# Optimization experiments

Hardware: AMD Instinct MI355X
Metric: run time of the kernel (lower is better)

The kernel has to match this reference:

```python
import jax, jax.numpy as jnp
import numpy as np

NEG_SLOPE = 0.2  # PyG GATConv leaky_relu slope


def _embed(feats, W1, b1, W2, b2, Wc, bc):
    # collapse_esm (two plain Linears, no activation) then linear_comb
    esm = feats[..., 24:] @ W1 + b1
    esm = esm @ W2 + b2
    x = jnp.concatenate([feats[..., :24], esm], axis=-1)
    return x @ Wc + bc


def _gat_conv(x, src, dst, n, W, a_src, a_dst, b, concat):
    # PyG GATConv: project, per-edge attention logits, softmax over incoming edges at dst,
    # weighted scatter-sum. Self loops already included in (src, dst).
    H, C = a_src.shape
    h = (x @ W).reshape(-1, H, C)                 # [N,H,C]
    s = (h * a_src).sum(-1)                       # [N,H]
    d = (h * a_dst).sum(-1)                       # [N,H]
    e = jax.nn.leaky_relu(s[src] + d[dst], NEG_SLOPE)  # [E,H]
    m = jax.ops.segment_max(e, dst, num_segments=n)
    e = jnp.exp(e - m[dst])
    z = jax.ops.segment_sum(e, dst, num_segments=n)
    alpha = e / z[dst]                            # [E,H]
    out = jax.ops.segment_sum(h[src] * alpha[:, :, None], dst, num_segments=n)  # [N,H,C]
    out = out.reshape(n, H * C) if concat else out.mean(axis=1)
    return out + b


def setup_inputs() -> dict:
    key = jax.random.key(0)
    ks = jax.random.split(key, 24)
    N, E, B, F = 100000, 3200000, 8, 50
    NF, M1, M2, M3, CH = 1304, 652, 326, 350, 32
    L, H, HID = 3, 8, 4
    f32 = jnp.float32
    inp = {
        "node_features": jax.random.normal(ks[0], (N, NF), f32),
        "edge_index": jax.random.randint(ks[1], (2, E), 0, N, dtype=jnp.int32),
        "edge_attr": jax.random.normal(ks[2], (E, 8), f32),
        "frag_emb": jax.random.normal(ks[3], (B, F, NF), f32),
        "W_esm1": jax.random.normal(ks[4], (NF - 24, M1), f32) / np.sqrt(NF - 24),
        "b_esm1": jnp.zeros((M1,), f32),
        "W_esm2": jax.random.normal(ks[5], (M1, M2), f32) / np.sqrt(M1),
        "b_esm2": jnp.zeros((M2,), f32),
        "W_comb": jax.random.normal(ks[6], (M3, CH), f32) / np.sqrt(M3),
        "b_comb": jnp.zeros((CH,), f32),
        "gat1_W": jax.random.normal(ks[7], (L, CH, H * HID), f32) / np.sqrt(CH),
        "gat1_asrc": jax.random.normal(ks[8], (L, H, HID), f32) * 0.1,
        "gat1_adst": jax.random.normal(ks[9], (L, H, HID), f32) * 0.1,
        "gat1_b": jnp.zeros((L, H * HID), f32),
        "gat2_W": jax.random.normal(ks[10], (L, H * HID, CH), f32) / np.sqrt(H * HID),
        "gat2_asrc": jax.random.normal(ks[11], (L, 1, CH), f32) * 0.1,
        "gat2_adst": jax.random.normal(ks[12], (L, 1, CH), f32) * 0.1,
        "gat2_b": jnp.zeros((L, CH), f32),
        "W_fin": jax.random.normal(ks[13], (CH, 1), f32) / np.sqrt(CH),
        "b_fin": jnp.zeros((1,), f32),
    }
    return inp


def reference(node_features, edge_index, edge_attr, frag_emb,
              W_esm1, b_esm1, W_esm2, b_esm2, W_comb, b_comb,
              gat1_W, gat1_asrc, gat1_adst, gat1_b,
              gat2_W, gat2_asrc, gat2_adst, gat2_b,
              W_fin, b_fin):
    N = node_features.shape[0]
    loop = jnp.arange(N, dtype=edge_index.dtype)
    src = jnp.concatenate([edge_index[0], loop])  # self loops (PyG default)
    dst = jnp.concatenate([edge_index[1], loop])

    x = _embed(node_features, W_esm1, b_esm1, W_esm2, b_esm2, W_comb, b_comb)  # [N,32]
    for i in range(gat1_W.shape[0]):
        x = _gat_conv(x, src, dst, N, gat1_W[i], gat1_asrc[i], gat1_adst[i], gat1_b[i], True)
        x = jax.nn.elu(x)
        x = _gat_conv(x, src, dst, N, gat2_W[i], gat2_asrc[i], gat2_adst[i], gat2_b[i], False)

    ys = _embed(frag_emb, W_esm1, b_esm1, W_esm2, b_esm2, W_comb, b_comb)  # [B,F,32]
    B, F, C = ys.shape
    xb = x.reshape(B, N // B, C)                      # equal-size graphs
    A = jax.nn.softmax(jnp.einsum('bnd,bfd->bnf', xb, ys), axis=-1)
    p = jnp.einsum('bnf,bfd->bnd', A, ys)             # [B,n,32]
    return jax.nn.sigmoid(p @ W_fin + b_fin).squeeze(-1)  # [B,n]
```

## Files before the change

### kernel.cpp

```cpp
#include <hip/hip_runtime.h>
#include <hip/hip_bf16.h>

#define NF 1304
#define M1 652
#define M2 326
#define CH 32
#define NHEAD1 8
#define HID1 4
#define NLAYER 3
#define FRAG 50
#define NBATCH 8
#define DPAD 32

static inline int ceil_div(int a, int b){ return (a + b - 1)/b; }

__device__ __forceinline__ unsigned short f2h(float f){
  _Float16 h = (_Float16)f;
  unsigned short u;
  __builtin_memcpy(&u, &h, 2);
  return u;
}
__device__ __forceinline__ float h2f(unsigned short u){
  _Float16 h;
  __builtin_memcpy(&h, &u, 2);
  return (float)h;
}

#define TM 64
#define TN 64
#define TKK 16
__global__ __launch_bounds__(256) void gemm_bias(
    const float* __restrict__ A, int lda,
    const float* __restrict__ B, int ldb,
    const float* __restrict__ bias,
    float* __restrict__ C, int ldc,
    int M, int N, int K, int acc)
{
  __shared__ float As[TKK][TM + 1];
  __shared__ float Bs[TKK][TN];
  int tid = threadIdx.x;
  int tx = tid & 15, ty = tid >> 4;
  int row0 = blockIdx.y * TM, col0 = blockIdx.x * TN;
  float c[4][4] = {};
  for (int k0 = 0; k0 < K; k0 += TKK) {
    #pragma unroll
    for (int p = 0; p < 4; ++p) {
      int r = (tid >> 4) + p * 16;
      int kk = tid & 15;
      int gr = row0 + r, gk = k0 + kk;
      float v = 0.f;
      if (gr < M && gk < K) v = A[(long long)gr * lda + gk];
      As[kk][r] = v;
    }
    #pragma unroll
    for (int p = 0; p < 4; ++p) {
      int kk = (tid >> 6) + p * 4;
      int cc = tid & 63;
      int gk = k0 + kk, gc = col0 + cc;
      float v = 0.f;
      if (gk < K && gc < N) v = B[(long long)gk * ldb + gc];
      Bs[kk][cc] = v;
    }
    __syncthreads();
    #pragma unroll
    for (int kk = 0; kk < TKK; ++kk) {
      float a[4], b[4];
      #pragma unroll
      for (int i = 0; i < 4; ++i) a[i] = As[kk][ty + 16 * i];
      #pragma unroll
      for (int j = 0; j < 4; ++j) b[j] = Bs[kk][tx + 16 * j];
      #pragma unroll
      for (int i = 0; i < 4; ++i)
        #pragma unroll
        for (int j = 0; j < 4; ++j)
          c[i][j] += a[i] * b[j];
    }
    __syncthreads();
  }
  #pragma unroll
  for (int i = 0; i < 4; ++i) {
    int gr = row0 + ty + 16 * i;
    if (gr >= M) continue;
    #pragma unroll
    for (int j = 0; j < 4; ++j) {
      int gc = col0 + tx + 16 * j;
      if (gc >= N) continue;
      float v = c[i][j];
      if (bias) v += bias[gc];
      if (acc) v += C[(long long)gr * ldc + gc];
      C[(long long)gr * ldc + gc] = v;
    }
  }
}

__global__ void fold_misc_kernel(const float* __restrict__ Wc, const float* __restrict__ T1,
                                 const float* __restrict__ b1, const float* __restrict__ b2,
                                 const float* __restrict__ bc,
                                 float* __restrict__ Wbig, float* __restrict__ bfold)
{
  int tid = threadIdx.x;
  for (int i = tid; i < 24 * CH; i += 256) Wbig[i] = Wc[i];
  if (tid < CH) {
    float v = bc[tid];
    for (int k = 0; k < M2; ++k) v += b2[k] * Wc[(24 + k) * CH + tid];
    for (int i = 0; i < M1; ++i) v += b1[i] * T1[i * CH + tid];
    bfold[tid] = v;
  }
}

#define EK 64
__global__ __launch_bounds__(256) void gemm_n32(
    const float* __restrict__ A, int M, int K,
    const float* __restrict__ W, const float* __restrict__ bias,
    float* __restrict__ C)
{
  __shared__ float As[64][65];
  __shared__ float Ws[EK][32];
  int tid = threadIdx.x;
  int row0 = blockIdx.x * 64;
  int tx = tid & 7, ty = tid >> 3;
  float c0[4] = {}, c1[4] = {};
  for (int k0 = 0; k0 < K; k0 += EK) {
    #pragma unroll
    for (int p = 0; p < 4; ++p) {
      int q = tid + p * 256;
      int r = q >> 4, c4 = (q & 15) * 4;
      int gr = row0 + r, gk = k0 + c4;
      float4 v = make_float4(0.f, 0.f, 0.f, 0.f);
      if (gr < M) {
        if (gk + 3 < K) v = *(const float4*)&A[(long long)gr * K + gk];
        else {
          float t[4] = {0.f, 0.f, 0.f, 0.f};
          for (int i = 0; i < 4; ++i) if (gk + i < K) t[i] = A[(long long)gr * K + gk + i];
          v = make_float4(t[0], t[1], t[2], t[3]);
        }
      }
      As[r][c4 + 0] = v.x; As[r][c4 + 1] = v.y; As[r][c4 + 2] = v.z; As[r][c4 + 3] = v.w;
    }
    #pragma unroll
    for (int p = 0; p < 2; ++p) {
      int q = tid + p * 256;
      int r = q >> 3, c4 = (q & 7) * 4;
      int gk = k0 + r;
      float4 v = make_float4(0.f, 0.f, 0.f, 0.f);
      if (gk < K) v = *(const float4*)&W[(long long)gk * 32 + c4];
      *(float4*)&Ws[r][c4] = v;
    }
    __syncthreads();
    #pragma unroll
    for (int kk = 0; kk < EK; ++kk) {
      float4 b = *(const float4*)&Ws[kk][tx * 4];
      float a0 = As[ty * 2][kk], a1 = As[ty * 2 + 1][kk];
      c0[0] += a0 * b.x; c0[1] += a0 * b.y; c0[2] += a0 * b.z; c0[3] += a0 * b.w;
      c1[0] += a1 * b.x; c1[1] += a1 * b.y; c1[2] += a1 * b.z; c1[3] += a1 * b.w;
    }
    __syncthreads();
  }
  float4 bb = *(const float4*)&bias[tx * 4];
  int gr0 = row0 + ty * 2;
  if (gr0 < M) {
    float4 v = make_float4(c0[0] + bb.x, c0[1] + bb.y, c0[2] + bb.z, c0[3] + bb.w);
    *(float4*)&C[(long long)gr0 * 32 + tx * 4] = v;
  }
  if (gr0 + 1 < M) {
    float4 v = make_float4(c1[0] + bb.x, c1[1] + bb.y, c1[2] + bb.z, c1[3] + bb.w);
    *(float4*)&C[(long long)(gr0 + 1) * 32 + tx * 4] = v;
  }
}

__global__ void zero_deg_kernel(int* __restrict__ degp, long long n)
{
  long long i = (long long)blockIdx.x * 256 + threadIdx.x;
  if (i < n) degp[i] = 0;
}
__global__ void rank_kernel(const int* __restrict__ ei, int E,
                            int* __restrict__ degp, int* __restrict__ rank)
{
  int e = blockIdx.x * 256 + threadIdx.x;
  if (e < E) rank[e] = atomicAdd(&degp[(long long)ei[E + e] * DPAD], 1);
}
__global__ void partial_kernel(const int* __restrict__ degp, int N, int* __restrict__ partial)
{
  __shared__ int sd[256];
  int i = blockIdx.x * 256 + threadIdx.x;
  sd[threadIdx.x] = (i < N) ? degp[(long long)i * DPAD] : 0;
  __syncthreads();
  for (int off = 128; off > 0; off >>= 1) {
    if (threadIdx.x < off) sd[threadIdx.x] += sd[threadIdx.x + off];
    __syncthreads();
  }
  if (threadIdx.x == 0) partial[blockIdx.x] = sd[0];
}
__global__ void scanp_kernel(int* __restrict__ partial, int NB)
{
  __shared__ int sd[512];
  int t = threadIdx.x;
  int v = (t < NB) ? partial[t] : 0;
  sd[t] = v;
  __syncthreads();
  for (int off = 1; off < 512; off <<= 1) {
    int u = (t >= off) ? sd[t - off] : 0;
    __syncthreads();
    sd[t] += u;
    __syncthreads();
  }
  if (t < NB) partial[t] = sd[t] - v;
}
__global__ void scan_final_kernel(const int* __restrict__ degp, int N,
                                  const int* __restrict__ partial,
                                  int* __restrict__ rowptr)
{
  __shared__ int sd[256];
  int i = blockIdx.x * 256 + threadIdx.x;
  int t = threadIdx.x;
  int v = (i < N) ? degp[(long long)i * DPAD] : 0;
  sd[t] = v;
  __syncthreads();
  for (int off = 1; off < 256; off <<= 1) {
    int u = (t >= off) ? sd[t - off] : 0;
    __syncthreads();
    sd[t] += u;
    __syncthreads();
  }
  if (i < N) {
    int excl = partial[blockIdx.x] + sd[t] - v;
    rowptr[i] = excl;
    if (i == N - 1) rowptr[N] = excl + v;
  }
}
__global__ void scatter_plain_kernel(const int* __restrict__ ei, int E,
                                     const int* __restrict__ rowptr,
                                     const int* __restrict__ rank,
                                     int* __restrict__ csr)
{
  int e = blockIdx.x * 256 + threadIdx.x;
  if (e >= E) return;
  int dn = ei[E + e];
  csr[rowptr[dn] + rank[e]] = ei[e];
}

template<int H, int C>
__global__ __launch_bounds__(256) void proj_sd_kernel(
    const float* __restrict__ x, const float* __restrict__ W,
    const float* __restrict__ adst,
    unsigned* __restrict__ hp, float* __restrict__ dv, int N)
{
  __shared__ float Ws[CH][CH];
  __shared__ float al[CH];
  int tid = threadIdx.x;
  for (int i = tid; i < CH * CH; i += 256) Ws[i >> 5][i & 31] = W[i];
  if (tid < CH) al[tid] = adst[tid];
  __syncthreads();
  int n = blockIdx.x * 256 + tid;
  if (n >= N) return;
  float xr[CH];
  #pragma unroll
  for (int j = 0; j < CH / 4; ++j) {
    float4 v = *(const float4*)&x[(long long)n * CH + j * 4];
    xr[j * 4] = v.x; xr[j * 4 + 1] = v.y; xr[j * 4 + 2] = v.z; xr[j * 4 + 3] = v.w;
  }
  float hr[CH] = {};
  #pragma unroll
  for (int c = 0; c < CH; ++c) {
    float xc = xr[c];
    #pragma unroll
    for (int j4 = 0; j4 < CH / 4; ++j4) {
      float4 w = *(const float4*)&Ws[c][j4 * 4];
      hr[j4 * 4] += xc * w.x; hr[j4 * 4 + 1] += xc * w.y;
      hr[j4 * 4 + 2] += xc * w.z; hr[j4 * 4 + 3] += xc * w.w;
    }
  }
  unsigned pk[16];
  #pragma unroll
  for (int j = 0; j < 16; ++j)
    pk[j] = (unsigned)f2h(hr[2 * j]) | ((unsigned)f2h(hr[2 * j + 1]) << 16);
  uint4* hq = (uint4*)&hp[(long long)n * 16];
  #pragma unroll
  for (int j = 0; j < 4; ++j)
    hq[j] = make_uint4(pk[4 * j], pk[4 * j + 1], pk[4 * j + 2], pk[4 * j + 3]);
  #pragma unroll
  for (int hh = 0; hh < H; ++hh) {
    float dd = 0.f;
    #pragma unroll
    for (int c = 0; c < C; ++c) dd += hr[hh * C + c] * al[hh * C + c];
    dv[(long long)n * H + hh] = dd;
  }
}

template<int H, int C>
__global__ __launch_bounds__(256) void gat_gather_kernel(
    const int* __restrict__ rowptr, const int* __restrict__ csr,
    const unsigned* __restrict__ hp, const float* __restrict__ asrc,
    const float* __restrict__ dv, const float* __restrict__ bias,
    float* __restrict__ xout, int N, int do_elu)
{
  int wid = threadIdx.x >> 6;
  int lane = threadIdx.x & 63;
  int n = blockIdx.x * 4 + wid;
  if (n >= N) return;
  int cpair = lane & 15;
  int slot = lane >> 4;
  int ch = cpair * 2;
  int hh = (C == HID1) ? (cpair >> 1) : 0;
  float a0 = asrc[ch], a1 = asrc[ch + 1];
  float dn = dv[(long long)n * H + hh];

  auto sred = [&](float p) {
    p += __shfl_xor(p, 1, 64);
    if (C == CH) {
      p += __shfl_xor(p, 2, 64);
      p += __shfl_xor(p, 4, 64);
      p += __shfl_xor(p, 8, 64);
    }
    return p;
  };

  float acc0 = 0.f, acc1 = 0.f, z = 0.f;
  {
    unsigned u = hp[(long long)n * 16 + cpair];
    float h0 = h2f((unsigned short)(u & 0xffff));
    float h1 = h2f((unsigned short)(u >> 16));
    float s = sred(h0 * a0 + h1 * a1);
    if (slot == 0) {
      float lg = s + dn;
      lg = lg > 0.f ? lg : 0.2f * lg;
      float w = expf(lg);
      z = w; acc0 = w * h0; acc1 = w * h1;
    }
  }
  int start = rowptr[n], end = rowptr[n + 1];
  for (int base = start; base < end; base += 64) {
    int b0 = base + slot * 16;
    int idx[16];
    #pragma unroll
    for (int t = 0; t < 16; ++t) {
      int p = b0 + t;
      idx[t] = (p < end) ? csr[p] : -1;
    }
    unsigned uu[16];
    #pragma unroll
    for (int t = 0; t < 16; ++t)
      uu[t] = (idx[t] >= 0) ? hp[(long long)idx[t] * 16 + cpair] : 0u;
    #pragma unroll
    for (int t = 0; t < 16; ++t) {
      float h0 = h2f((unsigned short)(uu[t] & 0xffff));
      float h1 = h2f((unsigned short)(uu[t] >> 16));
      float s = sred(h0 * a0 + h1 * a1);
      float lg = s + dn;
      lg = lg > 0.f ? lg : 0.2f * lg;
      float w = (idx[t] >= 0) ? expf(lg) : 0.f;
      z += w;
      acc0 += w * h0;
      acc1 += w * h1;
    }
  }
  acc0 += __shfl_xor(acc0, 16, 64); acc0 += __shfl_xor(acc0, 32, 64);
  acc1 += __shfl_xor(acc1, 16, 64); acc1 += __shfl_xor(acc1, 32, 64);
  z    += __shfl_xor(z, 16, 64);    z    += __shfl_xor(z, 32, 64);
  if (slot == 0) {
    float v0 = acc0 / z + bias[ch];
    float v1 = acc1 / z + bias[ch + 1];
    if (do_elu) {
      v0 = v0 > 0.f ? v0 : (expf(v0) - 1.f);
      v1 = v1 > 0.f ? v1 : (expf(v1) - 1.f);
    }
    *(float2*)&xout[(long long)n * 32 + ch] = make_float2(v0, v1);
  }
}

__global__ __launch_bounds__(256) void pool_kernel(
    const float* __restrict__ x, const float* __restrict__ ys,
    const float* __restrict__ Wfin, const float* __restrict__ bfin,
    float* __restrict__ out, int NB)
{
  __shared__ float ysl[FRAG][CH];
  __shared__ float tl[FRAG];
  int b = blockIdx.y;
  int tid = threadIdx.x;
  for (int idx = tid; idx < FRAG * CH; idx += 256)
    ysl[idx >> 5][idx & 31] = ys[(long long)b * FRAG * CH + idx];
  __syncthreads();
  if (tid < FRAG) {
    float t = 0.f;
    #pragma unroll
    for (int dd = 0; dd < CH; ++dd) t += ysl[tid][dd] * Wfin[dd];
    tl[tid] = t;
  }
  __syncthreads();
  int n = blockIdx.x * 256 + tid;
  if (n >= NB) return;
  const float* xr = x + ((long long)b * NB + n) * CH;
  float xreg[CH];
  #pragma unroll
  for (int dd = 0; dd < CH; ++dd) xreg[dd] = xr[dd];
  float mx = -1e30f;
  for (int f = 0; f < FRAG; ++f) {
    float l = 0.f;
    #pragma unroll
    for (int dd = 0; dd < CH; ++dd) l += xreg[dd] * ysl[f][dd];
    mx = fmaxf(mx, l);
  }
  float se = 0.f, sw = 0.f;
  for (int f = 0; f < FRAG; ++f) {
    float l = 0.f;
    #pragma unroll
    for (int dd = 0; dd < CH; ++dd) l += xreg[dd] * ysl[f][dd];
    float e = expf(l - mx);
    se += e; sw += e * tl[f];
  }
  float logit = sw / se + bfin[0];
  out[(long long)b * NB + n] = 1.f / (1.f + expf(-logit));
}

extern "C" void kernel_launch(void* const* d_in, const int* in_sizes, int n_in,
                              void* d_out, int out_size, void* d_ws, size_t ws_size,
                              hipStream_t stream)
{
  const float* feats = (const float*)d_in[0];
  const int*   ei    = (const int*)d_in[1];
  const float* frag  = (const float*)d_in[3];
  const float* W1    = (const float*)d_in[4];
  const float* b1    = (const float*)d_in[5];
  const float* W2    = (const float*)d_in[6];
  const float* b2    = (const float*)d_in[7];
  const float* Wc    = (const float*)d_in[8];
  const float* bc    = (const float*)d_in[9];
  const float* g1W   = (const float*)d_in[10];
  const float* g1as  = (const float*)d_in[11];
  const float* g1ad  = (const float*)d_in[12];
  const float* g1b   = (const float*)d_in[13];
  const float* g2W   = (const float*)d_in[14];
  const float* g2as  = (const float*)d_in[15];
  const float* g2ad  = (const float*)d_in[16];
  const float* g2b   = (const float*)d_in[17];
  const float* Wfin  = (const float*)d_in[18];
  const float* bfin  = (const float*)d_in[19];

  const int N  = in_sizes[0] / NF;
  const int E  = in_sizes[1] / 2;
  const int BF = in_sizes[3] / NF;
  const int NB = N / NBATCH;

  char* ws = (char*)d_ws;
  size_t off = 0;
  auto walloc = [&](size_t bytes) -> void* {
    void* p = ws + off;
    off += (bytes + 255) & ~(size_t)255;
    return p;
  };
  float*    T1     = (float*)walloc((size_t)M1 * CH * 4);
  float*    Wbig   = (float*)walloc((size_t)NF * CH * 4);
  float*    bfold  = (float*)walloc((size_t)CH * 4);
  float*    x0     = (float*)walloc((size_t)N * CH * 4);
  float*    x1     = (float*)walloc((size_t)N * CH * 4);
  unsigned* hbuf   = (unsigned*)walloc((size_t)N * 16 * 4);
  float*    dbuf   = (float*)walloc((size_t)N * NHEAD1 * 4);
  float*    ysb    = (float*)walloc((size_t)BF * CH * 4);
  int*      degp   = (int*)walloc((size_t)N * DPAD * 4);
  int*      rowptr = (int*)walloc((size_t)(N + 1) * 4);
  int*      rank   = (int*)walloc((size_t)E * 4);
  int*      part   = (int*)walloc((size_t)512 * 4);
  int*      csr    = (int*)walloc((size_t)E * 4);
  (void)ws_size; (void)n_in; (void)out_size;

  {
    dim3 g1(1, ceil_div(M1, TM));
    gemm_bias<<<g1, 256, 0, stream>>>(W2, M2, Wc + 24 * CH, CH, nullptr, T1, CH,
                                      M1, CH, M2, 0);
    dim3 g2(1, ceil_div(NF - 24, TM));
    gemm_bias<<<g2, 256, 0, stream>>>(W1, M1, T1, CH, nullptr, Wbig + 24 * CH, CH,
                                      NF - 24, CH, M1, 0);
    fold_misc_kernel<<<1, 256, 0, stream>>>(Wc, T1, b1, b2, bc, Wbig, bfold);
  }

  {
    long long npad = (long long)N * DPAD;
    int nb = ceil_div(N, 256);
    zero_deg_kernel<<<(int)((npad + 255) / 256), 256, 0, stream>>>(degp, npad);
    rank_kernel<<<ceil_div(E, 256), 256, 0, stream>>>(ei, E, degp, rank);
    partial_kernel<<<nb, 256, 0, stream>>>(degp, N, part);
    scanp_kernel<<<1, 512, 0, stream>>>(part, nb);
    scan_final_kernel<<<nb, 256, 0, stream>>>(degp, N, part, rowptr);
    scatter_plain_kernel<<<ceil_div(E, 256), 256, 0, stream>>>(ei, E, rowptr, rank, csr);
  }

  gemm_n32<<<ceil_div(N, 64), 256, 0, stream>>>(feats, N, NF, Wbig, bfold, x0);
  gemm_n32<<<ceil_div(BF, 64), 256, 0, stream>>>(frag, BF, NF, Wbig, bfold, ysb);

  auto conv = [&](const float* xin, float* xout, const float* W, const float* as_,
                  const float* ad_, const float* bias, int H, int do_elu) {
    if (H == NHEAD1) {
      proj_sd_kernel<NHEAD1, HID1><<<ceil_div(N, 256), 256, 0, stream>>>(
          xin, W, ad_, hbuf, dbuf, N);
      gat_gather_kernel<NHEAD1, HID1><<<ceil_div(N, 4), 256, 0, stream>>>(
          rowptr, csr, hbuf, as_, dbuf, bias, xout, N, do_elu);
    } else {
      proj_sd_kernel<1, CH><<<ceil_div(N, 256), 256, 0, stream>>>(
          xin, W, ad_, hbuf, dbuf, N);
      gat_gather_kernel<1, CH><<<ceil_div(N, 4), 256, 0, stream>>>(
          rowptr, csr, hbuf, as_, dbuf, bias, xout, N, do_elu);
    }
  };

  for (int l = 0; l < NLAYER; ++l) {
    conv(x0, x1, g1W + l * CH * CH, g1as + l * NHEAD1 * HID1, g1ad + l * NHEAD1 * HID1,
         g1b + l * CH, NHEAD1, 1);
    conv(x1, x0, g2W + l * CH * CH, g2as + l * CH, g2ad + l * CH,
         g2b + l * CH, 1, 0);
  }

  pool_kernel<<<dim3(ceil_div(NB, 256), NBATCH), 256, 0, stream>>>(
      x0, ysb, Wfin, bfin, (float*)d_out, NB);
}
```

Measured before the change: 1.497 ms.

## Restructure GAT gather: 4 channels per lane, 8 edge slots, coalesced index load

The GAT gather kernel now gives each lane 4 fp16 channels, loaded as one 8-byte uint2, instead of 2. Each wave therefore processes 8 edges at a time rather than 4. Neighbor indices are read once per 64-edge chunk with a single coalesced load and handed out through wave shuffles, replacing the old per-slot serial index loads. The aim is more memory-level parallelism per load, fewer shuffle reductions per edge, and less index-load latency, at the cost of more registers per lane.

```diff
diff --git a/kernel.cpp b/kernel.cpp
--- a/kernel.cpp
+++ b/kernel.cpp
@@ -298,73 +298,86 @@
   int lane = threadIdx.x & 63;
   int n = blockIdx.x * 4 + wid;
   if (n >= N) return;
-  int cpair = lane & 15;
-  int slot = lane >> 4;
-  int ch = cpair * 2;
-  int hh = (C == HID1) ? (cpair >> 1) : 0;
-  float a0 = asrc[ch], a1 = asrc[ch + 1];
+  int q = lane & 7;
+  int slot = lane >> 3;
+  int ch = q * 4;
+  int hh = (C == HID1) ? q : 0;
+  float a0 = asrc[ch], a1 = asrc[ch + 1], a2 = asrc[ch + 2], a3 = asrc[ch + 3];
   float dn = dv[(long long)n * H + hh];
 
   auto sred = [&](float p) {
-    p += __shfl_xor(p, 1, 64);
     if (C == CH) {
+      p += __shfl_xor(p, 1, 64);
       p += __shfl_xor(p, 2, 64);
       p += __shfl_xor(p, 4, 64);
-      p += __shfl_xor(p, 8, 64);
     }
     return p;
   };
 
-  float acc0 = 0.f, acc1 = 0.f, z = 0.f;
+  float acc0 = 0.f, acc1 = 0.f, acc2 = 0.f, acc3 = 0.f, z = 0.f;
   {
-    unsigned u = hp[(long long)n * 16 + cpair];
-    float h0 = h2f((unsigned short)(u & 0xffff));
-    float h1 = h2f((unsigned short)(u >> 16));
-    float s = sred(h0 * a0 + h1 * a1);
+    uint2 u = *(const uint2*)&hp[(long long)n * 16 + q * 2];
+    float h0 = h2f((unsigned short)(u.x & 0xffff));
+    float h1 = h2f((unsigned short)(u.x >> 16));
+    float h2v = h2f((unsigned short)(u.y & 0xffff));
+    float h3 = h2f((unsigned short)(u.y >> 16));
+    float s = sred(h0 * a0 + h1 * a1 + h2v * a2 + h3 * a3);
     if (slot == 0) {
       float lg = s + dn;
       lg = lg > 0.f ? lg : 0.2f * lg;
       float w = expf(lg);
-      z = w; acc0 = w * h0; acc1 = w * h1;
+      z = w; acc0 = w * h0; acc1 = w * h1; acc2 = w * h2v; acc3 = w * h3;
     }
   }
   int start = rowptr[n], end = rowptr[n + 1];
   for (int base = start; base < end; base += 64) {
-    int b0 = base + slot * 16;
-    int idx[16];
-    #pragma unroll
-    for (int t = 0; t < 16; ++t) {
-      int p = b0 + t;
-      idx[t] = (p < end) ? csr[p] : -1;
-    }
-    unsigned uu[16];
-    #pragma unroll
-    for (int t = 0; t < 16; ++t)
-      uu[t] = (idx[t] >= 0) ? hp[(long long)idx[t] * 16 + cpair] : 0u;
-    #pragma unroll
-    for (int t = 0; t < 16; ++t) {
-      float h0 = h2f((unsigned short)(uu[t] & 0xffff));
-      float h1 = h2f((unsigned short)(uu[t] >> 16));
-      float s = sred(h0 * a0 + h1 * a1);
-      float lg = s + dn;
-      lg = lg > 0.f ? lg : 0.2f * lg;
-      float w = (idx[t] >= 0) ? expf(lg) : 0.f;
-      z += w;
-      acc0 += w * h0;
-      acc1 += w * h1;
-    }
-  }
-  acc0 += __shfl_xor(acc0, 16, 64); acc0 += __shfl_xor(acc0, 32, 64);
-  acc1 += __shfl_xor(acc1, 16, 64); acc1 += __shfl_xor(acc1, 32, 64);
-  z    += __shfl_xor(z, 16, 64);    z    += __shfl_xor(z, 32, 64);
+    int m = end - base; if (m > 64) m = 64;
+    int idx = (base + lane < end) ? csr[base + lane] : 0;
+    #pragma unroll
+    for (int half = 0; half < 2; ++half) {
+      int si[4]; bool vld[4]; uint2 u[4];
+      #pragma unroll
+      for (int t = 0; t < 4; ++t) {
+        int k = slot + (half * 4 + t) * 8;
+        si[t] = __shfl(idx, k, 64);
+        vld[t] = (k < m);
+      }
+      #pragma unroll
+      for (int t = 0; t < 4; ++t)
+        u[t] = vld[t] ? *(const uint2*)&hp[(long long)si[t] * 16 + q * 2]
+                      : make_uint2(0u, 0u);
+      #pragma unroll
+      for (int t = 0; t < 4; ++t) {
+        float h0 = h2f((unsigned short)(u[t].x & 0xffff));
+        float h1 = h2f((unsigned short)(u[t].x >> 16));
+        float h2v = h2f((unsigned short)(u[t].y & 0xffff));
+        float h3 = h2f((unsigned short)(u[t].y >> 16));
+        float s = sred(h0 * a0 + h1 * a1 + h2v * a2 + h3 * a3);
+        float lg = s + dn;
+        lg = lg > 0.f ? lg : 0.2f * lg;
+        float w = vld[t] ? expf(lg) : 0.f;
+        z += w;
+        acc0 += w * h0; acc1 += w * h1; acc2 += w * h2v; acc3 += w * h3;
+      }
+    }
+  }
+  acc0 += __shfl_xor(acc0, 8, 64); acc0 += __shfl_xor(acc0, 16, 64); acc0 += __shfl_xor(acc0, 32, 64);
+  acc1 += __shfl_xor(acc1, 8, 64); acc1 += __shfl_xor(acc1, 16, 64); acc1 += __shfl_xor(acc1, 32, 64);
+  acc2 += __shfl_xor(acc2, 8, 64); acc2 += __shfl_xor(acc2, 16, 64); acc2 += __shfl_xor(acc2, 32, 64);
+  acc3 += __shfl_xor(acc3, 8, 64); acc3 += __shfl_xor(acc3, 16, 64); acc3 += __shfl_xor(acc3, 32, 64);
+  z    += __shfl_xor(z, 8, 64);    z    += __shfl_xor(z, 16, 64);    z    += __shfl_xor(z, 32, 64);
   if (slot == 0) {
     float v0 = acc0 / z + bias[ch];
     float v1 = acc1 / z + bias[ch + 1];
+    float v2 = acc2 / z + bias[ch + 2];
+    float v3 = acc3 / z + bias[ch + 3];
     if (do_elu) {
       v0 = v0 > 0.f ? v0 : (expf(v0) - 1.f);
       v1 = v1 > 0.f ? v1 : (expf(v1) - 1.f);
-    }
-    *(float2*)&xout[(long long)n * 32 + ch] = make_float2(v0, v1);
+      v2 = v2 > 0.f ? v2 : (expf(v2) - 1.f);
+      v3 = v3 > 0.f ? v3 : (expf(v3) - 1.f);
+    }
+    *(float4*)&xout[(long long)n * 32 + ch] = make_float4(v0, v1, v2, v3);
   }
 }
 
```

Measured after the change: 1.458 ms. 2.6% less time.
